# Performance work log

Hardware: AMD Instinct MI355X
Metric: run time of the kernel (lower is better)

The kernel has to match this reference:

```python
import math
import jax, jax.numpy as jnp
import numpy as np

NH, NKV, HD = 16, 8, 128  # n_heads, n_kv_heads, head_dim from config

def setup_inputs() -> dict:
    key = jax.random.key(0)
    ks = jax.random.split(key, 5)
    B, T, D = 2, 2048, 2048
    KV = NKV * HD  # 1024
    s = 1.0 / math.sqrt(D)
    return {
        "x": jax.random.normal(ks[0], (B, T, D), dtype=jnp.float32),
        "Wq": jax.random.normal(ks[1], (D, D), dtype=jnp.float32) * s,
        "Wk": jax.random.normal(ks[2], (KV, D), dtype=jnp.float32) * s,
        "Wv": jax.random.normal(ks[3], (KV, D), dtype=jnp.float32) * s,
        "Wo": jax.random.normal(ks[4], (D, D), dtype=jnp.float32) * s,
    }

def reference(x, Wq, Wk, Wv, Wo):
    B, T, D = x.shape
    groups = NH // NKV
    scale = 1.0 / math.sqrt(HD)
    # Projections (torch Linear: y = x @ W.T)
    q = (x @ Wq.T).reshape(B, T, NH, HD).transpose(0, 2, 1, 3)    # [B, nh, T, hd]
    k = (x @ Wk.T).reshape(B, T, NKV, HD).transpose(0, 2, 1, 3)   # [B, nkv, T, hd]
    v = (x @ Wv.T).reshape(B, T, NKV, HD).transpose(0, 2, 1, 3)   # [B, nkv, T, hd]
    kv_state = jnp.concatenate([k, v], axis=-1)                    # [B, nkv, T, 2*hd]
    # GQA: replicate kv heads (repeat_interleave along head dim)
    k = jnp.repeat(k, groups, axis=1)                              # [B, nh, T, hd]
    v = jnp.repeat(v, groups, axis=1)
    scores = jnp.einsum('bhqd,bhkd->bhqk', q, k) * scale           # [B, nh, T, T]
    causal = jnp.tril(jnp.ones((T, T), dtype=bool))
    scores = jnp.where(causal, scores, jnp.finfo(scores.dtype).min)
    probs = jax.nn.softmax(scores, axis=-1)
    attn = jnp.einsum('bhqk,bhkd->bhqd', probs, v)                 # [B, nh, T, hd]
    attn = attn.transpose(0, 2, 1, 3).reshape(B, T, NH * HD)
    output = attn @ Wo.T
    return (output, kv_state)
```

## Files before the change

kernel.cpp:

```cpp
#include <hip/hip_runtime.h>
#include <hip/hip_bf16.h>
#include <cstdint>
#include <cstddef>

#define DEV __device__ __forceinline__

typedef __attribute__((ext_vector_type(8))) short short8;
typedef __attribute__((ext_vector_type(4))) float f32x4;
typedef __attribute__((ext_vector_type(8))) __bf16 bf16x8;

DEV unsigned short f2bf(float f) {
    unsigned u = __builtin_bit_cast(unsigned, f);
    u += 0x7fffu + ((u >> 16) & 1u);
    return (unsigned short)(u >> 16);
}

DEV unsigned short f2bf_hw(float f) {
    return __builtin_bit_cast(unsigned short, (__bf16)f);
}

DEV f32x4 mfma16(short8 a, short8 b, f32x4 c) {
    return __builtin_amdgcn_mfma_f32_16x16x32_bf16(
        __builtin_bit_cast(bf16x8, a), __builtin_bit_cast(bf16x8, b), c, 0, 0, 0);
}

#define GLD_TO_LDS16(g, l)                                                  \
    __builtin_amdgcn_global_load_lds(                                       \
        (const __attribute__((address_space(1))) void*)(g),                 \
        (__attribute__((address_space(3))) void*)(l), 16, 0, 0)

__global__ void cvt_all(const float* __restrict__ x,  const float* __restrict__ wq,
                        const float* __restrict__ wk, const float* __restrict__ wv,
                        const float* __restrict__ wo,
                        unsigned short* __restrict__ xb,  unsigned short* __restrict__ wqb,
                        unsigned short* __restrict__ wkb, unsigned short* __restrict__ wvb,
                        unsigned short* __restrict__ wob) {
    constexpr int NX = 1048576, NQ = 524288, NK = 262144, NV = 262144, NO = 524288;
    constexpr int C1 = NX, C2 = C1 + NQ, C3 = C2 + NK, C4 = C3 + NV, C5 = C4 + NO;
    int i = blockIdx.x * blockDim.x + threadIdx.x;
    int stride = gridDim.x * blockDim.x;
    for (; i < C5; i += stride) {
        const float* s;
        unsigned short* d;
        int j;
        if (i < C1)      { s = x;  d = xb;  j = i; }
        else if (i < C2) { s = wq; d = wqb; j = i - C1; }
        else if (i < C3) { s = wk; d = wkb; j = i - C2; }
        else if (i < C4) { s = wv; d = wvb; j = i - C3; }
        else             { s = wo; d = wob; j = i - C4; }
        const f32x4* sp = (const f32x4*)(s + (size_t)j * 8);
        f32x4 a = sp[0], bq = sp[1];
        short8 o;
        o[0] = (short)f2bf(a[0]);  o[1] = (short)f2bf(a[1]);
        o[2] = (short)f2bf(a[2]);  o[3] = (short)f2bf(a[3]);
        o[4] = (short)f2bf(bq[0]); o[5] = (short)f2bf(bq[1]);
        o[6] = (short)f2bf(bq[2]); o[7] = (short)f2bf(bq[3]);
        *(short8*)(d + (size_t)j * 8) = o;
    }
}

__global__ __launch_bounds__(256) void transpose_v(
    const unsigned short* __restrict__ src, unsigned short* __restrict__ dst) {
    __shared__ __align__(16) unsigned short tile[64 * 64];
    const int t0 = blockIdx.x * 64;
    const int d0 = blockIdx.y * 64;
    const int b  = blockIdx.z;
    const int tid = threadIdx.x;
#pragma unroll
    for (int p = 0; p < 2; ++p) {
        int ch = tid + p * 256;
        int it = ch >> 3, ic8 = ch & 7;
        short8 v = *(const short8*)(src + (size_t)(b * 2048 + t0 + it) * 1024 + d0 + ic8 * 8);
        *(short8*)&tile[it * 64 + ((ic8 ^ (it & 7)) << 3)] = v;
    }
    __syncthreads();
#pragma unroll
    for (int p = 0; p < 2; ++p) {
        int ch = tid + p * 256;
        int od = ch >> 3, ot8 = ch & 7;
        short8 v;
#pragma unroll
        for (int j = 0; j < 8; ++j) {
            int t = ot8 * 8 + j;
            v[j] = (short)tile[t * 64 + ((((od >> 3) ^ (t & 7)) << 3) | (od & 7))];
        }
        *(short8*)(dst + (size_t)(b * 1024 + d0 + od) * 2048 + t0 + ot8 * 8) = v;
    }
}

__global__ __launch_bounds__(256) void gemm_qkv(
    const unsigned short* __restrict__ A,
    const unsigned short* __restrict__ Wq, const unsigned short* __restrict__ Wk,
    const unsigned short* __restrict__ Wv,
    unsigned short* __restrict__ Qo, unsigned short* __restrict__ Ko,
    unsigned short* __restrict__ Vo, float* __restrict__ kvf) {
    constexpr int K = 2048, BM = 128, BN = 128, BK = 32;
    __shared__ __align__(16) unsigned short sA[2][BM * BK];
    __shared__ __align__(16) unsigned short sB[2][BN * BK];

    const int tid = threadIdx.x;
    const int lane = tid & 63;
    const int wid = tid >> 6;
    const int wr = wid >> 1, wc = wid & 1;
    const int m0 = blockIdx.y * BM, n0 = blockIdx.x * BN;
    const int KT = K / BK;

    const unsigned short* Bp;
    unsigned short* Co;
    int c0, ostr, doff = 0;
    bool iskv = false;
    if (n0 < 2048)      { Bp = Wq + (size_t)n0 * K;          Co = Qo; c0 = n0;        ostr = 2048; }
    else if (n0 < 3072) { Bp = Wk + (size_t)(n0 - 2048) * K; Co = Ko; c0 = n0 - 2048; ostr = 1024; iskv = true; doff = 0; }
    else                { Bp = Wv + (size_t)(n0 - 3072) * K; Co = Vo; c0 = n0 - 3072; ostr = 1024; iskv = true; doff = 128; }

    auto stage = [&](int buf, int kt) {
#pragma unroll
        for (int p = 0; p < 2; ++p) {
            int ch = tid + p * 256;
            int r = ch >> 2, c = (ch & 3) * 8;
            GLD_TO_LDS16(A + (size_t)(m0 + r) * K + kt * BK + c, &sA[buf][ch * 8]);
        }
#pragma unroll
        for (int p = 0; p < 2; ++p) {
            int ch = tid + p * 256;
            int r = ch >> 2, c = (ch & 3) * 8;
            GLD_TO_LDS16(Bp + (size_t)r * K + kt * BK + c, &sB[buf][ch * 8]);
        }
    };

    f32x4 acc[4][4];
#pragma unroll
    for (int i = 0; i < 4; ++i)
#pragma unroll
        for (int j = 0; j < 4; ++j) acc[i][j] = (f32x4)0.f;

    stage(0, 0);
    int cur = 0;
    const int lrow = lane & 15, lko = (lane >> 4) * 8;
    for (int kt = 0; kt < KT; ++kt) {
        __syncthreads();
        if (kt + 1 < KT) stage(cur ^ 1, kt + 1);
        short8 af[4], bfr[4];
#pragma unroll
        for (int mi = 0; mi < 4; ++mi)
            af[mi] = *(const short8*)&sA[cur][(wr * 64 + mi * 16 + lrow) * BK + lko];
#pragma unroll
        for (int ni = 0; ni < 4; ++ni)
            bfr[ni] = *(const short8*)&sB[cur][(wc * 64 + ni * 16 + lrow) * BK + lko];
#pragma unroll
        for (int mi = 0; mi < 4; ++mi)
#pragma unroll
            for (int ni = 0; ni < 4; ++ni)
                acc[mi][ni] = mfma16(af[mi], bfr[ni], acc[mi][ni]);
        cur ^= 1;
    }

    const int lrow4 = (lane >> 4) * 4, lcol = lane & 15;
#pragma unroll
    for (int mi = 0; mi < 4; ++mi) {
#pragma unroll
        for (int ni = 0; ni < 4; ++ni) {
#pragma unroll
            for (int r = 0; r < 4; ++r) {
                int row = m0 + wr * 64 + mi * 16 + lrow4 + r;
                int col = c0 + wc * 64 + ni * 16 + lcol;
                float v = acc[mi][ni][r];
                Co[(size_t)row * ostr + col] = f2bf(v);
                if (iskv) {
                    int b = row >> 11, t = row & 2047;
                    int kh = col >> 7, d = col & 127;
                    kvf[((size_t)(b * 8 + kh) * 2048 + t) * 256 + doff + d] = v;
                }
            }
        }
    }
}

__global__ __launch_bounds__(256) void gemm_bt_f32(
    const unsigned short* __restrict__ A, const unsigned short* __restrict__ Bm,
    float* __restrict__ Cf, int M, int N, int K) {
    constexpr int BM = 128, BN = 128, BK = 32;
    __shared__ __align__(16) unsigned short sA[2][BM * BK];
    __shared__ __align__(16) unsigned short sB[2][BN * BK];

    const int tid = threadIdx.x;
    const int lane = tid & 63;
    const int wid = tid >> 6;
    const int wr = wid >> 1, wc = wid & 1;
    const int m0 = blockIdx.y * BM, n0 = blockIdx.x * BN;
    const int KT = K / BK;

    auto stage = [&](int buf, int kt) {
#pragma unroll
        for (int p = 0; p < 2; ++p) {
            int ch = tid + p * 256;
            int r = ch >> 2, c = (ch & 3) * 8;
            GLD_TO_LDS16(A + (size_t)(m0 + r) * K + kt * BK + c, &sA[buf][ch * 8]);
        }
#pragma unroll
        for (int p = 0; p < 2; ++p) {
            int ch = tid + p * 256;
            int r = ch >> 2, c = (ch & 3) * 8;
            GLD_TO_LDS16(Bm + (size_t)(n0 + r) * K + kt * BK + c, &sB[buf][ch * 8]);
        }
    };

    f32x4 acc[4][4];
#pragma unroll
    for (int i = 0; i < 4; ++i)
#pragma unroll
        for (int j = 0; j < 4; ++j) acc[i][j] = (f32x4)0.f;

    stage(0, 0);
    int cur = 0;
    const int lrow = lane & 15, lko = (lane >> 4) * 8;
    for (int kt = 0; kt < KT; ++kt) {
        __syncthreads();
        if (kt + 1 < KT) stage(cur ^ 1, kt + 1);
        short8 af[4], bfr[4];
#pragma unroll
        for (int mi = 0; mi < 4; ++mi)
            af[mi] = *(const short8*)&sA[cur][(wr * 64 + mi * 16 + lrow) * BK + lko];
#pragma unroll
        for (int ni = 0; ni < 4; ++ni)
            bfr[ni] = *(const short8*)&sB[cur][(wc * 64 + ni * 16 + lrow) * BK + lko];
#pragma unroll
        for (int mi = 0; mi < 4; ++mi)
#pragma unroll
            for (int ni = 0; ni < 4; ++ni)
                acc[mi][ni] = mfma16(af[mi], bfr[ni], acc[mi][ni]);
        cur ^= 1;
    }

    const int lrow4 = (lane >> 4) * 4, lcol = lane & 15;
#pragma unroll
    for (int mi = 0; mi < 4; ++mi)
#pragma unroll
        for (int ni = 0; ni < 4; ++ni)
#pragma unroll
            for (int r = 0; r < 4; ++r) {
                int row = m0 + wr * 64 + mi * 16 + lrow4 + r;
                int col = n0 + wc * 64 + ni * 16 + lcol;
                Cf[(size_t)row * N + col] = acc[mi][ni][r];
            }
}

__global__ __launch_bounds__(512, 4) void attn_fwd(
    const unsigned short* __restrict__ Qb, const unsigned short* __restrict__ Kb,
    const unsigned short* __restrict__ Vtg, unsigned short* __restrict__ Ob) {
    constexpr int T = 2048, DQ = 2048, DKV = 1024, HD = 128;
    constexpr float SC2 = 0.08838834764831845f * 1.4426950408889634f;
    constexpr float SHIFT = 8.0f * 1.4426950408889634f;
    __shared__ __align__(16) unsigned short Ks[64 * 136];
    __shared__ __align__(16) unsigned short Vs[128 * 72];
    __shared__ __align__(16) unsigned short Ps[8][16 * 72];

    const int bx = blockIdx.x, kh = blockIdx.y, b = blockIdx.z;
    const int qtile = b ? (31 - bx) : bx;
    const int tid = threadIdx.x, lane = tid & 63, w = tid >> 6;
    const int h = kh * 2 + (w >> 2);
    const int lrow = lane & 15, lg = lane >> 4;
    const int qt0 = qtile * 64;
    const int qrow0 = qt0 + (w & 3) * 16;
    const size_t bT = (size_t)b * T;

    short8 qf[4];
    {
        const unsigned short* qbase = Qb + (bT + qrow0 + lrow) * DQ + h * HD + lg * 8;
#pragma unroll
        for (int kc = 0; kc < 4; ++kc) qf[kc] = *(const short8*)(qbase + kc * 32);
    }

    int kr[2], kc8[2], vd[2], vk8[2];
#pragma unroll
    for (int p = 0; p < 2; ++p) {
        int ch = tid + p * 512;
        kr[p] = ch >> 4;  kc8[p] = ch & 15;
        vd[p] = ch >> 3;  vk8[p] = ch & 7;
    }
    const unsigned short* kbase = Kb + bT * DKV + kh * HD;
    const unsigned short* vbase = Vtg + (size_t)(b * 8 + kh) * 128 * T;
    short8 kreg[2], vreg[2];
    auto gload = [&](int kt) {
#pragma unroll
        for (int p = 0; p < 2; ++p) {
            kreg[p] = *(const short8*)(kbase + (size_t)(kt * 64 + kr[p]) * DKV + kc8[p] * 8);
            vreg[p] = *(const short8*)(vbase + (size_t)vd[p] * T + kt * 64 + vk8[p] * 8);
        }
    };
    auto lwrite = [&]() {
#pragma unroll
        for (int p = 0; p < 2; ++p) {
            *(short8*)&Ks[kr[p] * 136 + kc8[p] * 8] = kreg[p];
            *(short8*)&Vs[vd[p] * 72 + vk8[p] * 8] = vreg[p];
        }
    };

    f32x4 o[8];
#pragma unroll
    for (int i = 0; i < 8; ++i) o[i] = (f32x4)0.f;
    float rsum[4] = {0.f, 0.f, 0.f, 0.f};

    const int nkt = qtile + 1;
    gload(0);
    for (int kt = 0; kt < nkt; ++kt) {
        const int kt0 = kt * 64;
        __syncthreads();
        lwrite();
        __syncthreads();
        if (kt + 1 < nkt) gload(kt + 1);

        f32x4 s[4];
        __builtin_amdgcn_s_setprio(1);
#pragma unroll
        for (int nt = 0; nt < 4; ++nt) {
            s[nt] = (f32x4)0.f;
#pragma unroll
            for (int kc = 0; kc < 4; ++kc) {
                short8 kf = *(const short8*)&Ks[(nt * 16 + lrow) * 136 + kc * 32 + lg * 8];
                s[nt] = mfma16(qf[kc], kf, s[nt]);
            }
        }
        __builtin_amdgcn_s_setprio(0);

        const int qabs = qrow0 + lg * 4;
        const bool diag = (kt == qtile);
#pragma unroll
        for (int nt = 0; nt < 4; ++nt) {
            int kcol = kt0 + nt * 16 + lrow;
#pragma unroll
            for (int r = 0; r < 4; ++r) {
                float p = exp2f(fmaf(s[nt][r], SC2, -SHIFT));
                if (diag && kcol > qabs + r) p = 0.f;
                rsum[r] += p;
                Ps[w][(lg * 4 + r) * 72 + nt * 16 + lrow] = f2bf_hw(p);
            }
        }

        __builtin_amdgcn_s_setprio(1);
#pragma unroll
        for (int kc2 = 0; kc2 < 2; ++kc2) {
            short8 pf = *(const short8*)&Ps[w][lrow * 72 + kc2 * 32 + lg * 8];
#pragma unroll
            for (int dt = 0; dt < 8; ++dt) {
                short8 vf = *(const short8*)&Vs[(dt * 16 + lrow) * 72 + kc2 * 32 + lg * 8];
                o[dt] = mfma16(pf, vf, o[dt]);
            }
        }
        __builtin_amdgcn_s_setprio(0);
    }

#pragma unroll
    for (int r = 0; r < 4; ++r) {
        float v = rsum[r];
        v += __shfl_xor(v, 1);
        v += __shfl_xor(v, 2);
        v += __shfl_xor(v, 4);
        v += __shfl_xor(v, 8);
        float inv = 1.f / v;
        int row = qrow0 + lg * 4 + r;
        unsigned short* obase = Ob + (bT + row) * DQ + h * HD + lrow;
#pragma unroll
        for (int dt = 0; dt < 8; ++dt) obase[dt * 16] = f2bf_hw(o[dt][r] * inv);
    }
}

extern "C" void kernel_launch(void* const* d_in, const int* in_sizes, int n_in,
                              void* d_out, int out_size, void* d_ws, size_t ws_size,
                              hipStream_t stream) {
    (void)in_sizes; (void)n_in; (void)out_size; (void)ws_size;
    const float* x  = (const float*)d_in[0];
    const float* Wq = (const float*)d_in[1];
    const float* Wk = (const float*)d_in[2];
    const float* Wv = (const float*)d_in[3];
    const float* Wo = (const float*)d_in[4];
    float* out = (float*)d_out;
    float* kv_out = out + (size_t)8388608;

    unsigned short* xb   = (unsigned short*)d_ws;
    unsigned short* wqb  = xb   + 8388608;
    unsigned short* wkb  = wqb  + 4194304;
    unsigned short* wvb  = wkb  + 2097152;
    unsigned short* wob  = wvb  + 2097152;
    unsigned short* qb   = wob  + 4194304;
    unsigned short* kb   = qb   + 8388608;
    unsigned short* vt   = kb   + 4194304;
    unsigned short* ab   = vt   + 4194304;
    unsigned short* vtmp = ab;

    cvt_all<<<dim3(2048), dim3(256), 0, stream>>>(x, Wq, Wk, Wv, Wo,
                                                  xb, wqb, wkb, wvb, wob);
    gemm_qkv<<<dim3(32, 32), 256, 0, stream>>>(xb, wqb, wkb, wvb, qb, kb, vtmp, kv_out);
    transpose_v<<<dim3(32, 16, 2), 256, 0, stream>>>(vtmp, vt);
    attn_fwd<<<dim3(32, 8, 2), 512, 0, stream>>>(qb, kb, vt, ab);
    gemm_bt_f32<<<dim3(16, 32), 256, 0, stream>>>(ab, wob, out, 4096, 2048, 2048);
}
```

Baseline: 265.2 us.

## Rewrite QKV GEMM with 256x256 tiles, 8 waves and interleaved prefetch

```diff
diff --git a/kernel.cpp b/kernel.cpp
--- a/kernel.cpp
+++ b/kernel.cpp
@@ -88,82 +88,133 @@
     }
 }
 
-__global__ __launch_bounds__(256) void gemm_qkv(
+__global__ __launch_bounds__(512, 2) void gemm_qkv_8p(
     const unsigned short* __restrict__ A,
     const unsigned short* __restrict__ Wq, const unsigned short* __restrict__ Wk,
     const unsigned short* __restrict__ Wv,
     unsigned short* __restrict__ Qo, unsigned short* __restrict__ Ko,
     unsigned short* __restrict__ Vo, float* __restrict__ kvf) {
-    constexpr int K = 2048, BM = 128, BN = 128, BK = 32;
-    __shared__ __align__(16) unsigned short sA[2][BM * BK];
-    __shared__ __align__(16) unsigned short sB[2][BN * BK];
-
-    const int tid = threadIdx.x;
-    const int lane = tid & 63;
-    const int wid = tid >> 6;
-    const int wr = wid >> 1, wc = wid & 1;
-    const int m0 = blockIdx.y * BM, n0 = blockIdx.x * BN;
-    const int KT = K / BK;
+    constexpr int K = 2048, BM = 256, KT = K / 64;
+    __shared__ __align__(16) unsigned short sA[2][2][BM][32];
+    __shared__ __align__(16) unsigned short sB[2][2][BM][32];
+
+    const int tid = threadIdx.x, lane = tid & 63, w = tid >> 6;
+    const int wm = w >> 2, wn = w & 3;
+    const int lrow = lane & 15, lg = lane >> 4;
+    const int m0 = blockIdx.y * BM, n0 = blockIdx.x * BM;
 
     const unsigned short* Bp;
     unsigned short* Co;
     int c0, ostr, doff = 0;
     bool iskv = false;
-    if (n0 < 2048)      { Bp = Wq + (size_t)n0 * K;          Co = Qo; c0 = n0;        ostr = 2048; }
-    else if (n0 < 3072) { Bp = Wk + (size_t)(n0 - 2048) * K; Co = Ko; c0 = n0 - 2048; ostr = 1024; iskv = true; doff = 0; }
-    else                { Bp = Wv + (size_t)(n0 - 3072) * K; Co = Vo; c0 = n0 - 3072; ostr = 1024; iskv = true; doff = 128; }
-
-    auto stage = [&](int buf, int kt) {
+    if (n0 < 2048)      { Bp = Wq + (size_t)n0 * K;        Co = Qo; c0 = n0;        ostr = 2048; }
+    else if (n0 < 3072) { Bp = Wk + (size_t)(n0-2048) * K; Co = Ko; c0 = n0 - 2048; ostr = 1024; iskv = true; }
+    else                { Bp = Wv + (size_t)(n0-3072) * K; Co = Vo; c0 = n0 - 3072; ostr = 1024; iskv = true; doff = 128; }
+
+    const unsigned short* Ab = A + (size_t)m0 * K;
+
+    auto stage = [&](const unsigned short* gcol, unsigned short* lds) {
 #pragma unroll
         for (int p = 0; p < 2; ++p) {
-            int ch = tid + p * 256;
-            int r = ch >> 2, c = (ch & 3) * 8;
-            GLD_TO_LDS16(A + (size_t)(m0 + r) * K + kt * BK + c, &sA[buf][ch * 8]);
-        }
-#pragma unroll
-        for (int p = 0; p < 2; ++p) {
-            int ch = tid + p * 256;
-            int r = ch >> 2, c = (ch & 3) * 8;
-            GLD_TO_LDS16(Bp + (size_t)r * K + kt * BK + c, &sB[buf][ch * 8]);
+            int ch = tid + p * 512;
+            int row = ch >> 2;
+            int slot = (ch & 3) ^ (row & 3);
+            GLD_TO_LDS16(gcol + (size_t)row * K + slot * 8, lds + ch * 8);
         }
     };
 
-    f32x4 acc[4][4];
-#pragma unroll
-    for (int i = 0; i < 4; ++i)
+    f32x4 acc[8][4];
+#pragma unroll
+    for (int i = 0; i < 8; ++i)
 #pragma unroll
         for (int j = 0; j < 4; ++j) acc[i][j] = (f32x4)0.f;
 
-    stage(0, 0);
-    int cur = 0;
-    const int lrow = lane & 15, lko = (lane >> 4) * 8;
+    const int xoff = (lg * 8) ^ ((lrow & 3) << 3);
+    const int arow0 = wm * 128 + lrow;
+    const int brow0 = wn * 64 + lrow;
+
+    stage(Ab,      &sA[0][0][0][0]);
+    stage(Bp,      &sB[0][0][0][0]);
+    stage(Ab + 32, &sA[0][1][0][0]);
+    stage(Bp + 32, &sB[0][1][0][0]);
+    asm volatile("s_waitcnt vmcnt(4)\n\ts_barrier" ::: "memory");
+
     for (int kt = 0; kt < KT; ++kt) {
-        __syncthreads();
-        if (kt + 1 < KT) stage(cur ^ 1, kt + 1);
-        short8 af[4], bfr[4];
-#pragma unroll
-        for (int mi = 0; mi < 4; ++mi)
-            af[mi] = *(const short8*)&sA[cur][(wr * 64 + mi * 16 + lrow) * BK + lko];
+        const int buf = kt & 1, nb = buf ^ 1;
+        const bool pre = (kt + 1 < KT);
+        const unsigned short* An = Ab + (kt + 1) * 64;
+        const unsigned short* Bn = Bp + (kt + 1) * 64;
+        short8 bfrag[4], afrag[4];
+
+        if (pre) stage(An, &sA[nb][0][0][0]);
 #pragma unroll
         for (int ni = 0; ni < 4; ++ni)
-            bfr[ni] = *(const short8*)&sB[cur][(wc * 64 + ni * 16 + lrow) * BK + lko];
+            bfrag[ni] = *(const short8*)(&sB[buf][0][brow0 + ni * 16][0] + xoff);
+#pragma unroll
+        for (int mi = 0; mi < 4; ++mi)
+            afrag[mi] = *(const short8*)(&sA[buf][0][arow0 + mi * 16][0] + xoff);
+        __builtin_amdgcn_s_setprio(1);
 #pragma unroll
         for (int mi = 0; mi < 4; ++mi)
 #pragma unroll
             for (int ni = 0; ni < 4; ++ni)
-                acc[mi][ni] = mfma16(af[mi], bfr[ni], acc[mi][ni]);
-        cur ^= 1;
+                acc[mi][ni] = mfma16(afrag[mi], bfrag[ni], acc[mi][ni]);
+        __builtin_amdgcn_s_setprio(0);
+
+        if (pre) stage(Bn, &sB[nb][0][0][0]);
+#pragma unroll
+        for (int mi = 0; mi < 4; ++mi)
+            afrag[mi] = *(const short8*)(&sA[buf][0][arow0 + 64 + mi * 16][0] + xoff);
+        __builtin_amdgcn_s_setprio(1);
+#pragma unroll
+        for (int mi = 0; mi < 4; ++mi)
+#pragma unroll
+            for (int ni = 0; ni < 4; ++ni)
+                acc[4 + mi][ni] = mfma16(afrag[mi], bfrag[ni], acc[4 + mi][ni]);
+        __builtin_amdgcn_s_setprio(0);
+
+        if (pre) asm volatile("s_waitcnt vmcnt(4)\n\ts_barrier" ::: "memory");
+        else     asm volatile("s_waitcnt vmcnt(0)\n\ts_barrier" ::: "memory");
+
+        if (pre) stage(An + 32, &sA[nb][1][0][0]);
+#pragma unroll
+        for (int ni = 0; ni < 4; ++ni)
+            bfrag[ni] = *(const short8*)(&sB[buf][1][brow0 + ni * 16][0] + xoff);
+#pragma unroll
+        for (int mi = 0; mi < 4; ++mi)
+            afrag[mi] = *(const short8*)(&sA[buf][1][arow0 + mi * 16][0] + xoff);
+        __builtin_amdgcn_s_setprio(1);
+#pragma unroll
+        for (int mi = 0; mi < 4; ++mi)
+#pragma unroll
+            for (int ni = 0; ni < 4; ++ni)
+                acc[mi][ni] = mfma16(afrag[mi], bfrag[ni], acc[mi][ni]);
+        __builtin_amdgcn_s_setprio(0);
+
+        if (pre) stage(Bn + 32, &sB[nb][1][0][0]);
+#pragma unroll
+        for (int mi = 0; mi < 4; ++mi)
+            afrag[mi] = *(const short8*)(&sA[buf][1][arow0 + 64 + mi * 16][0] + xoff);
+        __builtin_amdgcn_s_setprio(1);
+#pragma unroll
+        for (int mi = 0; mi < 4; ++mi)
+#pragma unroll
+            for (int ni = 0; ni < 4; ++ni)
+                acc[4 + mi][ni] = mfma16(afrag[mi], bfrag[ni], acc[4 + mi][ni]);
+        __builtin_amdgcn_s_setprio(0);
+
+        if (pre) asm volatile("s_waitcnt vmcnt(4)\n\ts_barrier" ::: "memory");
     }
 
     const int lrow4 = (lane >> 4) * 4, lcol = lane & 15;
 #pragma unroll
-    for (int mi = 0; mi < 4; ++mi) {
+    for (int mi = 0; mi < 8; ++mi) {
 #pragma unroll
         for (int ni = 0; ni < 4; ++ni) {
 #pragma unroll
             for (int r = 0; r < 4; ++r) {
-                int row = m0 + wr * 64 + mi * 16 + lrow4 + r;
-                int col = c0 + wc * 64 + ni * 16 + lcol;
+                int row = m0 + wm * 128 + mi * 16 + lrow4 + r;
+                int col = c0 + wn * 64 + ni * 16 + lcol;
                 float v = acc[mi][ni][r];
                 Co[(size_t)row * ostr + col] = f2bf(v);
                 if (iskv) {
@@ -390,7 +441,7 @@
 
     cvt_all<<<dim3(2048), dim3(256), 0, stream>>>(x, Wq, Wk, Wv, Wo,
                                                   xb, wqb, wkb, wvb, wob);
-    gemm_qkv<<<dim3(32, 32), 256, 0, stream>>>(xb, wqb, wkb, wvb, qb, kb, vtmp, kv_out);
+    gemm_qkv_8p<<<dim3(16, 16), 512, 0, stream>>>(xb, wqb, wkb, wvb, qb, kb, vtmp, kv_out);
     transpose_v<<<dim3(32, 16, 2), 256, 0, stream>>>(vtmp, vt);
     attn_fwd<<<dim3(32, 8, 2), 512, 0, stream>>>(qb, kb, vt, ab);
     gemm_bt_f32<<<dim3(16, 32), 256, 0, stream>>>(ab, wob, out, 4096, 2048, 2048);
```

Result: faster. 225.1 us (-15.1%).
